# Kernel optimization log

Hardware: AMD Instinct MI355X
Metric: run time of the kernel (lower is better)

## Reference

```python
import jax, jax.numpy as jnp
import numpy as np
import math

B, S, D, DFF = 32, 2048, 512, 512


def setup_inputs() -> dict:
    key = jax.random.key(0)
    ks = jax.random.split(key, 10)
    s = 1.0 / math.sqrt(D)
    inp = {
        "x": jax.random.normal(ks[0], (B, S, D), dtype=jnp.float32),
        "Wq": jax.random.uniform(ks[1], (DFF, D), jnp.float32, -s, s),
        "bq": jax.random.uniform(ks[2], (DFF,), jnp.float32, -s, s),
        "Wk": jax.random.uniform(ks[3], (DFF, D), jnp.float32, -s, s),
        "bk": jax.random.uniform(ks[4], (DFF,), jnp.float32, -s, s),
        "Wv": jax.random.uniform(ks[5], (DFF, D), jnp.float32, -s, s),
        "bv": jax.random.uniform(ks[6], (DFF,), jnp.float32, -s, s),
        "Wt": jax.random.uniform(ks[7], (1, S), jnp.float32, -1.0 / math.sqrt(S), 1.0 / math.sqrt(S)),
        "bt": jax.random.uniform(ks[8], (1,), jnp.float32, -1.0 / math.sqrt(S), 1.0 / math.sqrt(S)),
    }
    return inp


def reference(x, Wq, bq, Wk, bk, Wv, bv, Wt, bt):
    # QKV projections: [B,S,DFF]
    q = jnp.einsum('bsd,fd->bsf', x, Wq) + bq
    k = jnp.einsum('bsd,fd->bsf', x, Wk) + bk
    v = jnp.einsum('bsd,fd->bsf', x, Wv) + bv
    # attention scores: [B,S,S]
    scores = jnp.einsum('bsf,btf->bst', q, k) / math.sqrt(DFF)
    # temporal reduction Linear(S->1): [B,S,1] -> [B,S]
    ta = jnp.einsum('bst,t->bs', scores, Wt[0]) + bt[0]
    # V-weighted sum: [B,DFF]
    latent = jnp.einsum('bsf,bs->bf', v, ta)
    return latent
```

## Files before the change

### kernel.cpp

```cpp
#include <hip/hip_runtime.h>

#define NB 32
#define NS 2048
#define ND 512
#define NFF 512
#define SCALE 0.044194173824159216f

__device__ __forceinline__ float dot4(float4 a, float4 b) {
    return a.x * b.x + a.y * b.y + a.z * b.z + a.w * b.w;
}

__device__ __forceinline__ float wave_reduce(float p) {
#pragma unroll
    for (int m = 1; m < 64; m <<= 1) p += __shfl_xor(p, m, 64);
    return p;
}

__global__ void k_swt(const float* __restrict__ Wt, float* __restrict__ swt) {
    __shared__ float red[256];
    float a = 0.f;
    for (int i = threadIdx.x; i < NS; i += 256) a += Wt[i];
    red[threadIdx.x] = a;
    __syncthreads();
    for (int off = 128; off > 0; off >>= 1) {
        if (threadIdx.x < off) red[threadIdx.x] += red[threadIdx.x + off];
        __syncthreads();
    }
    if (threadIdx.x == 0) *swt = red[0];
}

__global__ void __launch_bounds__(256) k_xw(const float* __restrict__ x,
                                            const float* __restrict__ Wt,
                                            float* __restrict__ xw) {
    const int b = blockIdx.x >> 5;
    const int chunk = blockIdx.x & 31;
    const int s0 = chunk * 64;
    const int t = threadIdx.x;
    const int col = t & 127;
    const int half = t >> 7;
    const float4* xb = (const float4*)(x + (size_t)b * NS * ND);
    float4 acc = make_float4(0.f, 0.f, 0.f, 0.f);
#pragma unroll 4
    for (int i = 0; i < 32; i++) {
        int s = s0 + half + 2 * i;
        float w = Wt[s];
        float4 v = xb[(size_t)s * 128 + col];
        acc.x += w * v.x; acc.y += w * v.y; acc.z += w * v.z; acc.w += w * v.w;
    }
    __shared__ float4 red[128];
    if (half == 1) red[col] = acc;
    __syncthreads();
    if (half == 0) {
        float4 o = red[col];
        float* dst = xw + b * ND + 4 * col;
        atomicAdd(dst + 0, acc.x + o.x);
        atomicAdd(dst + 1, acc.y + o.y);
        atomicAdd(dst + 2, acc.z + o.z);
        atomicAdd(dst + 3, acc.w + o.w);
    }
}

__global__ void __launch_bounds__(256) k_kw(const float* __restrict__ xw,
                                            const float* __restrict__ Wk,
                                            const float* __restrict__ bk,
                                            const float* __restrict__ swt,
                                            float* __restrict__ kw) {
    const int gw = blockIdx.x * 4 + (threadIdx.x >> 6);
    const int lane = threadIdx.x & 63;
    const int b = gw >> 5;
    const int f0 = (gw & 31) * 16;
    const float4* xw4 = (const float4*)(xw + b * ND);
    const float4 xa = xw4[lane];
    const float4 xc = xw4[64 + lane];
    const float sw = *swt;
#pragma unroll 4
    for (int j = 0; j < 16; j++) {
        int f = f0 + j;
        const float4* wr = (const float4*)(Wk + (size_t)f * ND);
        float p = dot4(xa, wr[lane]) + dot4(xc, wr[64 + lane]);
        p = wave_reduce(p);
        if (lane == 0) kw[b * NFF + f] = p + bk[f] * sw;
    }
}

__global__ void __launch_bounds__(512) k_wqkw(const float* __restrict__ kw,
                                              const float* __restrict__ Wq,
                                              const float* __restrict__ bq,
                                              const float* __restrict__ bt,
                                              float* __restrict__ wqs,
                                              float* __restrict__ cb2) {
    const int b = blockIdx.x;
    const int t = threadIdx.x;
    __shared__ float kwl[NFF];
    kwl[t] = kw[b * NFF + t];
    __syncthreads();
    float acc = 0.f;
#pragma unroll 8
    for (int f = 0; f < NFF; f++) acc += kwl[f] * Wq[(size_t)f * ND + t];
    wqs[b * ND + t] = acc * SCALE;
    __shared__ float red[512];
    red[t] = kwl[t] * bq[t];
    __syncthreads();
    for (int off = 256; off > 0; off >>= 1) {
        if (t < off) red[t] += red[t + off];
        __syncthreads();
    }
    if (t == 0) cb2[b] = red[0] * SCALE + bt[0];
}

__global__ void __launch_bounds__(256) k_ta_xt(const float* __restrict__ x,
                                               const float* __restrict__ wqs,
                                               const float* __restrict__ cb2,
                                               float* __restrict__ xt,
                                               float* __restrict__ st) {
    const int b = blockIdx.x >> 5;
    const int chunk = blockIdx.x & 31;
    const int wave = threadIdx.x >> 6;
    const int lane = threadIdx.x & 63;
    const float4* xb = (const float4*)(x + (size_t)b * NS * ND);
    const float4* wq4 = (const float4*)(wqs + b * ND);
    const float4 w0 = wq4[lane];
    const float4 w1 = wq4[64 + lane];
    const float c = cb2[b];
    float4 a0 = make_float4(0.f, 0.f, 0.f, 0.f);
    float4 a1 = make_float4(0.f, 0.f, 0.f, 0.f);
    float sta = 0.f;
#pragma unroll 2
    for (int i = 0; i < 16; i++) {
        int s = chunk * 64 + wave * 16 + i;
        float4 v0 = xb[(size_t)s * 128 + lane];
        float4 v1 = xb[(size_t)s * 128 + 64 + lane];
        float p = dot4(v0, w0) + dot4(v1, w1);
        p = wave_reduce(p);
        float ta = p + c;
        a0.x += ta * v0.x; a0.y += ta * v0.y; a0.z += ta * v0.z; a0.w += ta * v0.w;
        a1.x += ta * v1.x; a1.y += ta * v1.y; a1.z += ta * v1.z; a1.w += ta * v1.w;
        sta += ta;
    }
    __shared__ float4 sh0[4][128];
    __shared__ float4 sh1[4][128];
    __shared__ float stw[4];
    sh0[wave][lane] = a0;
    sh0[wave][64 + lane] = a1;
    sh1[wave][lane] = a1;
    if (lane == 0) stw[wave] = sta;
    __syncthreads();
    const int t = threadIdx.x;
    if (t < 64) {
        float4 s0 = sh0[0][t], s1 = sh0[1][t], s2 = sh0[2][t], s3 = sh0[3][t];
        float* dst = xt + b * ND + 4 * t;
        atomicAdd(dst + 0, s0.x + s1.x + s2.x + s3.x);
        atomicAdd(dst + 1, s0.y + s1.y + s2.y + s3.y);
        atomicAdd(dst + 2, s0.z + s1.z + s2.z + s3.z);
        atomicAdd(dst + 3, s0.w + s1.w + s2.w + s3.w);
    } else if (t < 128) {
        int l = t - 64;
        float4 s0 = sh1[0][l], s1 = sh1[1][l], s2 = sh1[2][l], s3 = sh1[3][l];
        float* dst = xt + b * ND + 256 + 4 * l;
        atomicAdd(dst + 0, s0.x + s1.x + s2.x + s3.x);
        atomicAdd(dst + 1, s0.y + s1.y + s2.y + s3.y);
        atomicAdd(dst + 2, s0.z + s1.z + s2.z + s3.z);
        atomicAdd(dst + 3, s0.w + s1.w + s2.w + s3.w);
    } else if (t == 128) {
        atomicAdd(st + b, stw[0] + stw[1] + stw[2] + stw[3]);
    }
}

__global__ void __launch_bounds__(256) k_latent(const float* __restrict__ xt,
                                                const float* __restrict__ Wv,
                                                const float* __restrict__ bv,
                                                const float* __restrict__ st,
                                                float* __restrict__ out) {
    const int gw = blockIdx.x * 4 + (threadIdx.x >> 6);
    const int lane = threadIdx.x & 63;
    const int b = gw >> 5;
    const int f0 = (gw & 31) * 16;
    const float4* xt4 = (const float4*)(xt + b * ND);
    const float4 xa = xt4[lane];
    const float4 xc = xt4[64 + lane];
    const float stb = st[b];
#pragma unroll 4
    for (int j = 0; j < 16; j++) {
        int f = f0 + j;
        const float4* wr = (const float4*)(Wv + (size_t)f * ND);
        float p = dot4(xa, wr[lane]) + dot4(xc, wr[64 + lane]);
        p = wave_reduce(p);
        if (lane == 0) out[b * NFF + f] = p + bv[f] * stb;
    }
}

extern "C" void kernel_launch(void* const* d_in, const int* in_sizes, int n_in,
                              void* d_out, int out_size, void* d_ws, size_t ws_size,
                              hipStream_t stream) {
    const float* x  = (const float*)d_in[0];
    const float* Wq = (const float*)d_in[1];
    const float* bq = (const float*)d_in[2];
    const float* Wk = (const float*)d_in[3];
    const float* bk = (const float*)d_in[4];
    const float* Wv = (const float*)d_in[5];
    const float* bv = (const float*)d_in[6];
    const float* Wt = (const float*)d_in[7];
    const float* bt = (const float*)d_in[8];
    float* out = (float*)d_out;

    float* w = (float*)d_ws;
    float* xw  = w;
    float* xt  = w + 16384;
    float* st  = w + 32768;
    float* swt = w + 32800;
    float* kw  = w + 32832;
    float* wqs = w + 49216;
    float* cb2 = w + 65600;

    hipMemsetAsync(d_ws, 0, (size_t)(32768 + 32) * sizeof(float), stream);

    k_swt<<<1, 256, 0, stream>>>(Wt, swt);
    k_xw<<<NB * 32, 256, 0, stream>>>(x, Wt, xw);
    k_kw<<<256, 256, 0, stream>>>(xw, Wk, bk, swt, kw);
    k_wqkw<<<NB, 512, 0, stream>>>(kw, Wq, bq, bt, wqs, cb2);
    k_ta_xt<<<NB * 32, 256, 0, stream>>>(x, wqs, cb2, xt, st);
    k_latent<<<256, 256, 0, stream>>>(xt, Wv, bv, st, out);
}
```

Measured before the change: 302.5 us.

## Replace atomics with per-block partials and fuse small kernels into fewer launches

Removes the workspace memset and all float atomicAdds by having k_xw and k_ta_xt write per-block partial sums, which the next kernel reduces. The Wt sum, Wk projection and Wq/bias contraction are fused into one 1024-thread-per-batch kernel, and k_latent now reduces the xt partials itself. This cuts the launch count from six kernels plus a memset to four kernels and avoids atomic contention. In exchange the fused kwq kernel runs on only 32 blocks, and every k_latent block redundantly reduces its batch's partials.

```diff
diff --git a/kernel.cpp b/kernel.cpp
--- a/kernel.cpp
+++ b/kernel.cpp
@@ -16,22 +16,9 @@
     return p;
 }
 
-__global__ void k_swt(const float* __restrict__ Wt, float* __restrict__ swt) {
-    __shared__ float red[256];
-    float a = 0.f;
-    for (int i = threadIdx.x; i < NS; i += 256) a += Wt[i];
-    red[threadIdx.x] = a;
-    __syncthreads();
-    for (int off = 128; off > 0; off >>= 1) {
-        if (threadIdx.x < off) red[threadIdx.x] += red[threadIdx.x + off];
-        __syncthreads();
-    }
-    if (threadIdx.x == 0) *swt = red[0];
-}
-
 __global__ void __launch_bounds__(256) k_xw(const float* __restrict__ x,
                                             const float* __restrict__ Wt,
-                                            float* __restrict__ xw) {
+                                            float* __restrict__ xwp) {
     const int b = blockIdx.x >> 5;
     const int chunk = blockIdx.x & 31;
     const int s0 = chunk * 64;
@@ -52,38 +39,15 @@
     __syncthreads();
     if (half == 0) {
         float4 o = red[col];
-        float* dst = xw + b * ND + 4 * col;
-        atomicAdd(dst + 0, acc.x + o.x);
-        atomicAdd(dst + 1, acc.y + o.y);
-        atomicAdd(dst + 2, acc.z + o.z);
-        atomicAdd(dst + 3, acc.w + o.w);
-    }
-}
-
-__global__ void __launch_bounds__(256) k_kw(const float* __restrict__ xw,
-                                            const float* __restrict__ Wk,
-                                            const float* __restrict__ bk,
-                                            const float* __restrict__ swt,
-                                            float* __restrict__ kw) {
-    const int gw = blockIdx.x * 4 + (threadIdx.x >> 6);
-    const int lane = threadIdx.x & 63;
-    const int b = gw >> 5;
-    const int f0 = (gw & 31) * 16;
-    const float4* xw4 = (const float4*)(xw + b * ND);
-    const float4 xa = xw4[lane];
-    const float4 xc = xw4[64 + lane];
-    const float sw = *swt;
-#pragma unroll 4
-    for (int j = 0; j < 16; j++) {
-        int f = f0 + j;
-        const float4* wr = (const float4*)(Wk + (size_t)f * ND);
-        float p = dot4(xa, wr[lane]) + dot4(xc, wr[64 + lane]);
-        p = wave_reduce(p);
-        if (lane == 0) kw[b * NFF + f] = p + bk[f] * sw;
-    }
-}
-
-__global__ void __launch_bounds__(512) k_wqkw(const float* __restrict__ kw,
+        o.x += acc.x; o.y += acc.y; o.z += acc.z; o.w += acc.w;
+        ((float4*)xwp)[(size_t)blockIdx.x * 128 + col] = o;
+    }
+}
+
+__global__ void __launch_bounds__(1024) k_kwq(const float* __restrict__ xwp,
+                                              const float* __restrict__ Wt,
+                                              const float* __restrict__ Wk,
+                                              const float* __restrict__ bk,
                                               const float* __restrict__ Wq,
                                               const float* __restrict__ bq,
                                               const float* __restrict__ bt,
@@ -91,28 +55,79 @@
                                               float* __restrict__ cb2) {
     const int b = blockIdx.x;
     const int t = threadIdx.x;
+    const int wv = t >> 6;
+    const int lane = t & 63;
+    __shared__ float xw[ND];
     __shared__ float kwl[NFF];
-    kwl[t] = kw[b * NFF + t];
-    __syncthreads();
-    float acc = 0.f;
+    __shared__ float part[2][ND];
+    __shared__ float cbred[16];
+    __shared__ float swt_s;
+
+    if (t < ND) {
+        float a = 0.f;
+        const float* p = xwp + (size_t)b * 32 * ND + t;
+#pragma unroll
+        for (int c = 0; c < 32; c++) a += p[c * ND];
+        xw[t] = a;
+    }
+    if (wv == 15) {
+        float a = 0.f;
+#pragma unroll
+        for (int j = 0; j < 32; j++) a += Wt[j * 64 + lane];
+        a = wave_reduce(a);
+        if (lane == 0) swt_s = a;
+    }
+    __syncthreads();
+
+    {
+        const float4* xw4 = (const float4*)xw;
+        const float4 xa = xw4[lane];
+        const float4 xc = xw4[64 + lane];
+        const float sw = swt_s;
+        float cbp = 0.f;
+#pragma unroll 4
+        for (int j = 0; j < 32; j++) {
+            int f = wv * 32 + j;
+            const float4* wr = (const float4*)(Wk + (size_t)f * ND);
+            float p = dot4(xa, wr[lane]) + dot4(xc, wr[64 + lane]);
+            p = wave_reduce(p);
+            if (lane == 0) {
+                float kf = p + bk[f] * sw;
+                kwl[f] = kf;
+                cbp += kf * bq[f];
+            }
+        }
+        if (lane == 0) cbred[wv] = cbp;
+    }
+    __syncthreads();
+
+    {
+        const int d = t & 511;
+        const int h = t >> 9;
+        float acc = 0.f;
+        const int f0 = h * 256;
 #pragma unroll 8
-    for (int f = 0; f < NFF; f++) acc += kwl[f] * Wq[(size_t)f * ND + t];
-    wqs[b * ND + t] = acc * SCALE;
-    __shared__ float red[512];
-    red[t] = kwl[t] * bq[t];
-    __syncthreads();
-    for (int off = 256; off > 0; off >>= 1) {
-        if (t < off) red[t] += red[t + off];
-        __syncthreads();
-    }
-    if (t == 0) cb2[b] = red[0] * SCALE + bt[0];
+        for (int j = 0; j < 256; j++) {
+            int f = f0 + j;
+            acc += kwl[f] * Wq[(size_t)f * ND + d];
+        }
+        part[h][d] = acc;
+        if (t == 0) {
+            float s = 0.f;
+#pragma unroll
+            for (int w = 0; w < 16; w++) s += cbred[w];
+            cb2[b] = SCALE * s + bt[0];
+        }
+    }
+    __syncthreads();
+    if (t < ND) wqs[b * ND + t] = SCALE * (part[0][t] + part[1][t]);
 }
 
 __global__ void __launch_bounds__(256) k_ta_xt(const float* __restrict__ x,
                                                const float* __restrict__ wqs,
                                                const float* __restrict__ cb2,
-                                               float* __restrict__ xt,
-                                               float* __restrict__ st) {
+                                               float* __restrict__ xtp,
+                                               float* __restrict__ stp) {
     const int b = blockIdx.x >> 5;
     const int chunk = blockIdx.x & 31;
     const int wave = threadIdx.x >> 6;
@@ -137,48 +152,68 @@
         a1.x += ta * v1.x; a1.y += ta * v1.y; a1.z += ta * v1.z; a1.w += ta * v1.w;
         sta += ta;
     }
-    __shared__ float4 sh0[4][128];
-    __shared__ float4 sh1[4][128];
+    __shared__ float4 sh0[4][64];
+    __shared__ float4 sh1[4][64];
     __shared__ float stw[4];
     sh0[wave][lane] = a0;
-    sh0[wave][64 + lane] = a1;
     sh1[wave][lane] = a1;
     if (lane == 0) stw[wave] = sta;
     __syncthreads();
     const int t = threadIdx.x;
+    float4* dst = (float4*)xtp + (size_t)blockIdx.x * 128;
     if (t < 64) {
         float4 s0 = sh0[0][t], s1 = sh0[1][t], s2 = sh0[2][t], s3 = sh0[3][t];
-        float* dst = xt + b * ND + 4 * t;
-        atomicAdd(dst + 0, s0.x + s1.x + s2.x + s3.x);
-        atomicAdd(dst + 1, s0.y + s1.y + s2.y + s3.y);
-        atomicAdd(dst + 2, s0.z + s1.z + s2.z + s3.z);
-        atomicAdd(dst + 3, s0.w + s1.w + s2.w + s3.w);
+        dst[t] = make_float4(s0.x + s1.x + s2.x + s3.x,
+                             s0.y + s1.y + s2.y + s3.y,
+                             s0.z + s1.z + s2.z + s3.z,
+                             s0.w + s1.w + s2.w + s3.w);
     } else if (t < 128) {
         int l = t - 64;
         float4 s0 = sh1[0][l], s1 = sh1[1][l], s2 = sh1[2][l], s3 = sh1[3][l];
-        float* dst = xt + b * ND + 256 + 4 * l;
-        atomicAdd(dst + 0, s0.x + s1.x + s2.x + s3.x);
-        atomicAdd(dst + 1, s0.y + s1.y + s2.y + s3.y);
-        atomicAdd(dst + 2, s0.z + s1.z + s2.z + s3.z);
-        atomicAdd(dst + 3, s0.w + s1.w + s2.w + s3.w);
+        dst[64 + l] = make_float4(s0.x + s1.x + s2.x + s3.x,
+                                  s0.y + s1.y + s2.y + s3.y,
+                                  s0.z + s1.z + s2.z + s3.z,
+                                  s0.w + s1.w + s2.w + s3.w);
     } else if (t == 128) {
-        atomicAdd(st + b, stw[0] + stw[1] + stw[2] + stw[3]);
-    }
-}
-
-__global__ void __launch_bounds__(256) k_latent(const float* __restrict__ xt,
+        stp[blockIdx.x] = stw[0] + stw[1] + stw[2] + stw[3];
+    }
+}
+
+__global__ void __launch_bounds__(256) k_latent(const float* __restrict__ xtp,
+                                                const float* __restrict__ stp,
                                                 const float* __restrict__ Wv,
                                                 const float* __restrict__ bv,
-                                                const float* __restrict__ st,
                                                 float* __restrict__ out) {
-    const int gw = blockIdx.x * 4 + (threadIdx.x >> 6);
-    const int lane = threadIdx.x & 63;
-    const int b = gw >> 5;
-    const int f0 = (gw & 31) * 16;
-    const float4* xt4 = (const float4*)(xt + b * ND);
+    const int b = blockIdx.x >> 3;
+    const int t = threadIdx.x;
+    __shared__ float xt[ND];
+    __shared__ float sts;
+    {
+        float a0 = 0.f, a1 = 0.f;
+        const float* p = xtp + (size_t)b * 32 * ND;
+#pragma unroll
+        for (int c = 0; c < 32; c++) {
+            a0 += p[c * ND + t];
+            a1 += p[c * ND + 256 + t];
+        }
+        xt[t] = a0;
+        xt[256 + t] = a1;
+        if (t == 0) {
+            float s = 0.f;
+            const float* sp = stp + b * 32;
+#pragma unroll
+            for (int c = 0; c < 32; c++) s += sp[c];
+            sts = s;
+        }
+    }
+    __syncthreads();
+    const int wv = t >> 6;
+    const int lane = t & 63;
+    const int f0 = ((blockIdx.x & 7) * 4 + wv) * 16;
+    const float4* xt4 = (const float4*)xt;
     const float4 xa = xt4[lane];
     const float4 xc = xt4[64 + lane];
-    const float stb = st[b];
+    const float stb = sts;
 #pragma unroll 4
     for (int j = 0; j < 16; j++) {
         int f = f0 + j;
@@ -204,20 +239,14 @@
     float* out = (float*)d_out;
 
     float* w = (float*)d_ws;
-    float* xw  = w;
-    float* xt  = w + 16384;
-    float* st  = w + 32768;
-    float* swt = w + 32800;
-    float* kw  = w + 32832;
-    float* wqs = w + 49216;
-    float* cb2 = w + 65600;
-
-    hipMemsetAsync(d_ws, 0, (size_t)(32768 + 32) * sizeof(float), stream);
-
-    k_swt<<<1, 256, 0, stream>>>(Wt, swt);
-    k_xw<<<NB * 32, 256, 0, stream>>>(x, Wt, xw);
-    k_kw<<<256, 256, 0, stream>>>(xw, Wk, bk, swt, kw);
-    k_wqkw<<<NB, 512, 0, stream>>>(kw, Wq, bq, bt, wqs, cb2);
-    k_ta_xt<<<NB * 32, 256, 0, stream>>>(x, wqs, cb2, xt, st);
-    k_latent<<<256, 256, 0, stream>>>(xt, Wv, bv, st, out);
-}
+    float* xwp = w;
+    float* xtp = w + 524288;
+    float* stp = w + 1048576;
+    float* wqs = w + 1049600;
+    float* cb2 = w + 1065984;
+
+    k_xw<<<NB * 32, 256, 0, stream>>>(x, Wt, xwp);
+    k_kwq<<<NB, 1024, 0, stream>>>(xwp, Wt, Wk, bk, Wq, bq, bt, wqs, cb2);
+    k_ta_xt<<<NB * 32, 256, 0, stream>>>(x, wqs, cb2, xtp, stp);
+    k_latent<<<256, 256, 0, stream>>>(xtp, stp, Wv, bv, out);
+}
```

Result: faster. 295.0 us (-2.5%).
